# Kernel optimization log

Measured on AMD Instinct MI355X. Metric: run time of the kernel, lower is better.

## Reference

```python
import jax, jax.numpy as jnp
import numpy as np

B, T, D = 4, 8192, 1024
C = 8.0


def setup_inputs() -> dict:
    key = jax.random.key(0)
    k1, k2, k3 = jax.random.split(key, 3)
    init_std = D ** (-0.5)
    x = jax.random.normal(k1, (B, T, D), dtype=jnp.float32)
    W_in = jax.random.truncated_normal(k2, -3.0, 3.0, (D, D), dtype=jnp.float32) * init_std
    W_gate = jax.random.truncated_normal(k3, -3.0, 3.0, (D, D), dtype=jnp.float32) * init_std
    b_in = jnp.zeros((D,), dtype=jnp.float32)
    b_gate = jnp.zeros((D,), dtype=jnp.float32)
    forget_lambda = jnp.linspace(-4.323, -9.0, D, dtype=jnp.float32)
    return {"x": x, "W_in": W_in, "b_in": b_in, "W_gate": W_gate,
            "b_gate": b_gate, "forget_lambda": forget_lambda}


def _combine(c1, c2):
    # linear recurrence h_t = a_t * h_{t-1} + b_t  (associative composition)
    a1, b1 = c1
    a2, b2 = c2
    return a1 * a2, a2 * b1 + b2


def reference(x, W_in, b_in, W_gate, b_gate, forget_lambda):
    # x: [B, T, D]
    input_gate = x @ W_in.T + b_in          # [B, T, D]
    recurrence_gate = x @ W_gate.T + b_gate  # [B, T, D]
    alpha = jnp.exp(-C * jax.nn.softplus(forget_lambda) * jax.nn.sigmoid(recurrence_gate))
    beta = jnp.sqrt(1.0 - alpha ** 2 + 1e-6)
    xbeta = beta * jax.nn.sigmoid(input_gate) * x
    # parallel scan of h_t = alpha_t * h_{t-1} + xbeta_t along sequence axis
    _, h = jax.lax.associative_scan(_combine, (alpha, xbeta), axis=1)
    return h
```

## Files before the change

### kernel.cpp

```cpp
#include <hip/hip_runtime.h>

typedef unsigned short u16;
typedef __attribute__((ext_vector_type(8))) short short8;
typedef __attribute__((ext_vector_type(4))) float f32x4;

#define T_SEQ 8192
#define DDIM 1024
#define BB 4
#define MM (BB * T_SEQ)
#define NC 128
#define CHUNK (T_SEQ / NC)
#define CHAINS (BB * DDIM)
#define NT 16

__device__ __forceinline__ float bf_lo(unsigned p) {
    union { unsigned u; float f; } v; v.u = p << 16; return v.f;
}
__device__ __forceinline__ float bf_hi(unsigned p) {
    union { unsigned u; float f; } v; v.u = p & 0xffff0000u; return v.f;
}
__device__ __forceinline__ float bf_u16(u16 p) {
    union { unsigned u; float f; } v; v.u = ((unsigned)p) << 16; return v.f;
}
__device__ __forceinline__ u16 f2bf(float f) {
    union { unsigned u; float f; } v; v.f = f;
    unsigned r = v.u + 0x7fffu + ((v.u >> 16) & 1u);
    return (u16)(r >> 16);
}
__device__ __forceinline__ float sigm(float z) {
    return __builtin_amdgcn_rcpf(1.0f + __expf(-z));
}
__device__ __forceinline__ void gld16(const u16* g, u16* l) {
    __builtin_amdgcn_global_load_lds((const __attribute__((address_space(1))) void*)g,
                                     (__attribute__((address_space(3))) void*)l, 16, 0, 0);
}

#define N4X (MM * DDIM / 4)
#define N4W (DDIM * DDIM / 4)
__global__ __launch_bounds__(256) void cvt_all(const float* __restrict__ x,
                                               const float* __restrict__ Wi,
                                               const float* __restrict__ Wg,
                                               u16* __restrict__ Xb,
                                               u16* __restrict__ Wib,
                                               u16* __restrict__ Wgb) {
    int i = blockIdx.x * 256 + threadIdx.x;
    const float* src; u16* dst; int j;
    if (i < N4X)            { src = x;  dst = Xb;  j = i; }
    else if (i < N4X + N4W) { src = Wi; dst = Wib; j = i - N4X; }
    else                    { src = Wg; dst = Wgb; j = i - N4X - N4W; }
    float4 v = ((const float4*)src)[j];
    ushort4 o;
    o.x = f2bf(v.x); o.y = f2bf(v.y); o.z = f2bf(v.z); o.w = f2bf(v.w);
    ((ushort4*)dst)[j] = o;
}


#define MROW(i_, av)                                                                   \
    acc[i_][0] = __builtin_amdgcn_mfma_f32_16x16x32_bf16(av, b0, acc[i_][0], 0, 0, 0); \
    acc[i_][1] = __builtin_amdgcn_mfma_f32_16x16x32_bf16(av, b1, acc[i_][1], 0, 0, 0); \
    acc[i_][2] = __builtin_amdgcn_mfma_f32_16x16x32_bf16(av, b2, acc[i_][2], 0, 0, 0); \
    acc[i_][3] = __builtin_amdgcn_mfma_f32_16x16x32_bf16(av, b3, acc[i_][3], 0, 0, 0);

#define MALL MROW(0, a0) MROW(1, a1) MROW(2, a2) MROW(3, a3) \
             MROW(4, a4) MROW(5, a5) MROW(6, a6) MROW(7, a7)

#define RDALL(kk)                                                            \
    b0 = LDB(kk, 0); b1 = LDB(kk, 1); b2 = LDB(kk, 2); b3 = LDB(kk, 3);      \
    a0 = LDA(kk, 0); a1 = LDA(kk, 1); a2 = LDA(kk, 2); a3 = LDA(kk, 3);      \
    a4 = LDA(kk, 4); a5 = LDA(kk, 5); a6 = LDA(kk, 6); a7 = LDA(kk, 7);

#define STA(buf, kh, rb, t_) gld16(gA + (size_t)(t_)*64 + (kh)*32 + (size_t)(rb)*128*DDIM, \
                                   &lds[(((buf)*2 + (kh))*1024 + (rb)*512 + tid)*8])
#define STB(buf, kh, hf, t_) gld16(((hf) ? gBg : gBi) + (size_t)(t_)*64 + (kh)*32,          \
                                   &lds[32768 + (((buf)*2 + (kh))*1024 + (hf)*512 + tid)*8])

#define LDA(kk, i) (*(const short8*)&lds[((cur*2 + (kk))*256 + arow0 + (i)*16)*32 + aoff])
#define LDB(kk, j) (*(const short8*)&lds[32768 + ((cur*2 + (kk))*256 + brow0 + (j)*16)*32 + aoff])

__global__ __launch_bounds__(512, 2)
void gemm_fused(const u16* __restrict__ X, const u16* __restrict__ Wi,
                const u16* __restrict__ Wg, const float* __restrict__ b_in,
                const float* __restrict__ b_gate, const float* __restrict__ lam,
                u16* __restrict__ Sg, u16* __restrict__ XBg) {
    const int bid = blockIdx.x;
    const int xcd = bid & 7;
    const int r = bid >> 3;
    const int n_tile = r & 7;
    const int m_tile = xcd * 16 + (r >> 3);
    const int tN0 = n_tile * 128;
    const int tM0 = m_tile * 256;

    const int tid = threadIdx.x;
    const int lane = tid & 63;
    const int w = tid >> 6;
    const int wm = w >> 2;
    const int wn = w & 3;
    const int gate = wn >> 1;
    const int wn_sub = wn & 1;

    __shared__ u16 lds[65536];

    const int srow = tid >> 2;
    const int c8log = (tid & 3) ^ ((tid >> 3) & 3);
    const u16* gA  = X  + (size_t)(tM0 + srow) * DDIM + c8log * 8;
    const u16* gBi = Wi + (size_t)(tN0 + srow) * DDIM + c8log * 8;
    const u16* gBg = Wg + (size_t)(tN0 + srow) * DDIM + c8log * 8;

    const int lm = lane & 15;
    const int aoff = (((lane >> 4) ^ ((lm >> 1) & 3))) * 8;
    const int arow0 = wm * 128 + lm;
    const int brow0 = gate * 128 + wn_sub * 64 + lm;

    f32x4 acc[8][4] = {};
    short8 a0, a1, a2, a3, a4, a5, a6, a7, b0, b1, b2, b3;

    STA(0, 0, 0, 0); STA(0, 0, 1, 0); STB(0, 0, 0, 0); STB(0, 0, 1, 0);
    STA(0, 1, 0, 0); STA(0, 1, 1, 0); STB(0, 1, 0, 0); STB(0, 1, 1, 0);
    asm volatile("s_waitcnt vmcnt(4)" ::: "memory");
    __builtin_amdgcn_s_barrier();

    for (int t = 0; t < NT - 1; ++t) {
        const int cur = t & 1, nb = cur ^ 1, tn = t + 1;
        RDALL(0)
        STA(nb, 0, 0, tn); STA(nb, 0, 1, tn); STB(nb, 0, 0, tn); STB(nb, 0, 1, tn);
        asm volatile("s_waitcnt vmcnt(4)" ::: "memory");
        __builtin_amdgcn_s_barrier();
        __builtin_amdgcn_s_setprio(1);
        MALL
        __builtin_amdgcn_s_setprio(0);
        __builtin_amdgcn_s_barrier();
        RDALL(1)
        STA(nb, 1, 0, tn); STA(nb, 1, 1, tn); STB(nb, 1, 0, tn); STB(nb, 1, 1, tn);
        asm volatile("s_waitcnt vmcnt(4)" ::: "memory");
        __builtin_amdgcn_s_barrier();
        __builtin_amdgcn_s_setprio(1);
        MALL
        __builtin_amdgcn_s_setprio(0);
        __builtin_amdgcn_s_barrier();
    }
    {
        const int cur = (NT - 1) & 1;
        RDALL(0)
        asm volatile("s_waitcnt vmcnt(0)" ::: "memory");
        __builtin_amdgcn_s_barrier();
        __builtin_amdgcn_s_setprio(1);
        MALL
        __builtin_amdgcn_s_setprio(0);
        __builtin_amdgcn_s_barrier();
        RDALL(1)
        __builtin_amdgcn_s_setprio(1);
        MALL
        __builtin_amdgcn_s_setprio(0);
        __builtin_amdgcn_s_barrier();
    }

    const int r0 = (lane >> 4) << 2;
    const int cb = lane & 15;
    if (gate) {
#pragma unroll
        for (int j = 0; j < 4; ++j) {
            const int colg = tN0 + wn_sub * 64 + j * 16 + cb;
            const int cl = wn_sub * 64 + j * 16 + cb;
            const float bj = b_gate[colg];
            const float nsp = -8.0f * log1pf(__expf(lam[colg]));
#pragma unroll
            for (int i = 0; i < 8; ++i) {
                const int rl0 = wm * 128 + i * 16 + r0;
#pragma unroll
                for (int rr = 0; rr < 4; ++rr) {
                    const int rl = rl0 + rr;
                    float s = nsp * sigm(acc[i][j][rr] + bj);
                    lds[rl * 128 + (cl ^ (((rl >> 2) & 7) << 4))] = f2bf(s);
                }
            }
        }
    } else {
#pragma unroll
        for (int j = 0; j < 4; ++j) {
            const int colg = tN0 + wn_sub * 64 + j * 16 + cb;
            const int cl = wn_sub * 64 + j * 16 + cb;
            const float bj = b_in[colg];
#pragma unroll
            for (int i = 0; i < 8; ++i) {
                const int rl0 = wm * 128 + i * 16 + r0;
#pragma unroll
                for (int rr = 0; rr < 4; ++rr) {
                    const int rl = rl0 + rr;
                    float p = sigm(acc[i][j][rr] + bj);
                    lds[32768 + rl * 128 + (cl ^ (((rl >> 2) & 7) << 4))] =
                        (u16)(p * 65535.0f + 0.5f);
                }
            }
        }
    }
    asm volatile("s_waitcnt lgkmcnt(0)" ::: "memory");
    __builtin_amdgcn_s_barrier();
    __builtin_amdgcn_sched_barrier(0);

    const int cc = tid & 15;
    const int rg0 = (tid >> 4) * 8;
#pragma unroll
    for (int k = 0; k < 8; ++k) {
        const int rl = rg0 + k;
        const int ch = (cc ^ (((rl >> 2) & 7) << 1)) * 8;
        short8 sv = *(const short8*)&lds[rl * 128 + ch];
        short8 pv = *(const short8*)&lds[32768 + rl * 128 + ch];
        const size_t go = (size_t)(tM0 + rl) * DDIM + tN0 + cc * 8;
        short8 xv = *(const short8*)&X[go];
        short8 ov;
#pragma unroll
        for (int e = 0; e < 8; ++e) {
            float s = bf_u16((u16)sv[e]);
            float p = (float)((u16)pv[e]) * (1.0f / 65535.0f);
            float xf = bf_u16((u16)xv[e]);
            float be = sqrtf(1.0f - __expf(2.0f * s) + 1e-6f);
            ov[e] = (short)f2bf(be * p * xf);
        }
        *(short8*)&Sg[go] = sv;
        *(short8*)&XBg[go] = ov;
    }
}

__global__ __launch_bounds__(256)
void scan_pass1(const u16* __restrict__ S, const u16* __restrict__ XB,
                float* __restrict__ AggA, float* __restrict__ AggB) {
    const int c = blockIdx.x, dblk = blockIdx.y, bq = blockIdx.z;
    const int d0 = dblk * 512 + threadIdx.x * 2;
    size_t base = ((size_t)(bq * T_SEQ + c * CHUNK)) * DDIM + d0;

    float A0 = 1.0f, B0 = 0.0f, A1 = 1.0f, B1 = 0.0f;
#pragma unroll 8
    for (int t = 0; t < CHUNK; t++) {
        unsigned sp = *(const unsigned*)(S + base);
        unsigned xp = *(const unsigned*)(XB + base);
        float a0 = __expf(bf_lo(sp));
        float a1 = __expf(bf_hi(sp));
        B0 = fmaf(a0, B0, bf_lo(xp)); A0 *= a0;
        B1 = fmaf(a1, B1, bf_hi(xp)); A1 *= a1;
        base += DDIM;
    }
    const int chain = bq * DDIM + d0;
    float2 av; av.x = A0; av.y = A1;
    float2 bv; bv.x = B0; bv.y = B1;
    *(float2*)(AggA + (size_t)c * CHAINS + chain) = av;
    *(float2*)(AggB + (size_t)c * CHAINS + chain) = bv;
}

__global__ __launch_bounds__(256)
void scan_pass2(const float* __restrict__ AggA, const float* __restrict__ AggB,
                float* __restrict__ H0) {
    const int chain = blockIdx.x * 256 + threadIdx.x;
    float p = 0.0f;
#pragma unroll 8
    for (int c = 0; c < NC; c++) {
        H0[(size_t)c * CHAINS + chain] = p;
        p = AggA[(size_t)c * CHAINS + chain] * p + AggB[(size_t)c * CHAINS + chain];
    }
}

__global__ __launch_bounds__(256)
void scan_pass3(const u16* __restrict__ S, const u16* __restrict__ XB,
                const float* __restrict__ H0, float* __restrict__ out) {
    const int c = blockIdx.x, dblk = blockIdx.y, bq = blockIdx.z;
    const int d0 = dblk * 512 + threadIdx.x * 2;
    size_t base = ((size_t)(bq * T_SEQ + c * CHUNK)) * DDIM + d0;
    const int chain = bq * DDIM + d0;

    float2 h = *(const float2*)(H0 + (size_t)c * CHAINS + chain);
#pragma unroll 8
    for (int t = 0; t < CHUNK; t++) {
        unsigned sp = *(const unsigned*)(S + base);
        unsigned xp = *(const unsigned*)(XB + base);
        float a0 = __expf(bf_lo(sp));
        float a1 = __expf(bf_hi(sp));
        h.x = fmaf(a0, h.x, bf_lo(xp));
        h.y = fmaf(a1, h.y, bf_hi(xp));
        *(float2*)(out + base) = h;
        base += DDIM;
    }
}

extern "C" void kernel_launch(void* const* d_in, const int* in_sizes, int n_in,
                              void* d_out, int out_size, void* d_ws, size_t ws_size,
                              hipStream_t stream) {
    const float* x   = (const float*)d_in[0];
    const float* Win = (const float*)d_in[1];
    const float* bin = (const float*)d_in[2];
    const float* Wg  = (const float*)d_in[3];
    const float* bg  = (const float*)d_in[4];
    const float* lam = (const float*)d_in[5];
    float* out = (float*)d_out;

    char* w = (char*)d_ws;
    u16* Wi_bf  = (u16*)(w);
    u16* Wg_bf  = (u16*)(w + (size_t)(2) * 1024 * 1024);
    u16* Sg     = (u16*)(w + (size_t)(4) * 1024 * 1024);
    u16* XBg    = (u16*)(w + (size_t)(68) * 1024 * 1024);
    float* AggA = (float*)(w + (size_t)(132) * 1024 * 1024);
    float* AggB = (float*)(w + (size_t)(134) * 1024 * 1024);
    float* H0   = (float*)(w + (size_t)(136) * 1024 * 1024);

    u16* Xbf = (u16*)d_out;

    cvt_all<<<dim3((N4X + 2 * N4W) / 256), dim3(256), 0, stream>>>(
        x, Win, Wg, Xbf, Wi_bf, Wg_bf);

    gemm_fused<<<dim3((DDIM / 128) * (MM / 256)), dim3(512), 0, stream>>>(
        Xbf, Wi_bf, Wg_bf, bin, bg, lam, Sg, XBg);

    scan_pass1<<<dim3(NC, 2, BB), dim3(256), 0, stream>>>(Sg, XBg, AggA, AggB);
    scan_pass2<<<dim3(CHAINS / 256), dim3(256), 0, stream>>>(AggA, AggB, H0);
    scan_pass3<<<dim3(NC, 2, BB), dim3(256), 0, stream>>>(Sg, XBg, H0, out);
}
```

Before: 477.4 us.

## Restructure GEMM main loop into 4-stage half-tile LDS ring buffer with prefetch depth 3

Replaces the double-buffered 64-wide K-tile loop, which used two barriers per half-tile, with a 4-slot ring of 32-wide K half-tiles. Global loads run three stages ahead and each iteration needs only one barrier. This aims to hide more global-load latency and cut synchronisation overhead in the fused input/gate GEMM. The wait counts and slot reuse have to be exactly right, otherwise a slot could be overwritten while another wave is still reading it.

```diff
diff --git a/kernel.cpp b/kernel.cpp
--- a/kernel.cpp
+++ b/kernel.cpp
@@ -12,6 +12,7 @@
 #define CHUNK (T_SEQ / NC)
 #define CHAINS (BB * DDIM)
 #define NT 16
+#define NHT 32
 
 __device__ __forceinline__ float bf_lo(unsigned p) {
     union { unsigned u; float f; } v; v.u = p << 16; return v.f;
@@ -64,18 +65,19 @@
 #define MALL MROW(0, a0) MROW(1, a1) MROW(2, a2) MROW(3, a3) \
              MROW(4, a4) MROW(5, a5) MROW(6, a6) MROW(7, a7)
 
-#define RDALL(kk)                                                            \
-    b0 = LDB(kk, 0); b1 = LDB(kk, 1); b2 = LDB(kk, 2); b3 = LDB(kk, 3);      \
-    a0 = LDA(kk, 0); a1 = LDA(kk, 1); a2 = LDA(kk, 2); a3 = LDA(kk, 3);      \
-    a4 = LDA(kk, 4); a5 = LDA(kk, 5); a6 = LDA(kk, 6); a7 = LDA(kk, 7);
-
-#define STA(buf, kh, rb, t_) gld16(gA + (size_t)(t_)*64 + (kh)*32 + (size_t)(rb)*128*DDIM, \
-                                   &lds[(((buf)*2 + (kh))*1024 + (rb)*512 + tid)*8])
-#define STB(buf, kh, hf, t_) gld16(((hf) ? gBg : gBi) + (size_t)(t_)*64 + (kh)*32,          \
-                                   &lds[32768 + (((buf)*2 + (kh))*1024 + (hf)*512 + tid)*8])
-
-#define LDA(kk, i) (*(const short8*)&lds[((cur*2 + (kk))*256 + arow0 + (i)*16)*32 + aoff])
-#define LDB(kk, j) (*(const short8*)&lds[32768 + ((cur*2 + (kk))*256 + brow0 + (j)*16)*32 + aoff])
+#define LDA_H(h_, i) (*(const short8*)&lds[((h_)&3)*8192 + (arow0 + (i)*16)*32 + aoff])
+#define LDB_H(h_, j) (*(const short8*)&lds[32768 + ((h_)&3)*8192 + (brow0 + (j)*16)*32 + aoff])
+
+#define RD_H(h_)                                                                       \
+    b0 = LDB_H(h_, 0); b1 = LDB_H(h_, 1); b2 = LDB_H(h_, 2); b3 = LDB_H(h_, 3);        \
+    a0 = LDA_H(h_, 0); a1 = LDA_H(h_, 1); a2 = LDA_H(h_, 2); a3 = LDA_H(h_, 3);        \
+    a4 = LDA_H(h_, 4); a5 = LDA_H(h_, 5); a6 = LDA_H(h_, 6); a7 = LDA_H(h_, 7);
+
+#define STA_H(h_, rb) gld16(gA + (size_t)(h_)*32 + (size_t)(rb)*128*DDIM,              \
+                            &lds[((h_)&3)*8192 + (rb)*4096 + tid*8])
+#define STB_H(h_, hf) gld16(((hf) ? gBg : gBi) + (size_t)(h_)*32,                      \
+                            &lds[32768 + ((h_)&3)*8192 + (hf)*4096 + tid*8])
+#define ST_H(h_) STA_H(h_, 0); STA_H(h_, 1); STB_H(h_, 0); STB_H(h_, 1);
 
 __global__ __launch_bounds__(512, 2)
 void gemm_fused(const u16* __restrict__ X, const u16* __restrict__ Wi,
@@ -114,45 +116,42 @@
     f32x4 acc[8][4] = {};
     short8 a0, a1, a2, a3, a4, a5, a6, a7, b0, b1, b2, b3;
 
-    STA(0, 0, 0, 0); STA(0, 0, 1, 0); STB(0, 0, 0, 0); STB(0, 0, 1, 0);
-    STA(0, 1, 0, 0); STA(0, 1, 1, 0); STB(0, 1, 0, 0); STB(0, 1, 1, 0);
-    asm volatile("s_waitcnt vmcnt(4)" ::: "memory");
-    __builtin_amdgcn_s_barrier();
-
-    for (int t = 0; t < NT - 1; ++t) {
-        const int cur = t & 1, nb = cur ^ 1, tn = t + 1;
-        RDALL(0)
-        STA(nb, 0, 0, tn); STA(nb, 0, 1, tn); STB(nb, 0, 0, tn); STB(nb, 0, 1, tn);
-        asm volatile("s_waitcnt vmcnt(4)" ::: "memory");
+    ST_H(0) ST_H(1) ST_H(2)
+
+    for (int h = 0; h < NHT - 3; ++h) {
+        asm volatile("s_waitcnt vmcnt(8)" ::: "memory");
         __builtin_amdgcn_s_barrier();
+        RD_H(h)
+        ST_H(h + 3)
         __builtin_amdgcn_s_setprio(1);
         MALL
         __builtin_amdgcn_s_setprio(0);
+    }
+    {
+        asm volatile("s_waitcnt vmcnt(8)" ::: "memory");
         __builtin_amdgcn_s_barrier();
-        RDALL(1)
-        STA(nb, 1, 0, tn); STA(nb, 1, 1, tn); STB(nb, 1, 0, tn); STB(nb, 1, 1, tn);
-        asm volatile("s_waitcnt vmcnt(4)" ::: "memory");
-        __builtin_amdgcn_s_barrier();
+        RD_H(29)
         __builtin_amdgcn_s_setprio(1);
         MALL
         __builtin_amdgcn_s_setprio(0);
+    }
+    {
+        asm volatile("s_waitcnt vmcnt(4)" ::: "memory");
         __builtin_amdgcn_s_barrier();
-    }
-    {
-        const int cur = (NT - 1) & 1;
-        RDALL(0)
-        asm volatile("s_waitcnt vmcnt(0)" ::: "memory");
-        __builtin_amdgcn_s_barrier();
+        RD_H(30)
         __builtin_amdgcn_s_setprio(1);
         MALL
         __builtin_amdgcn_s_setprio(0);
+    }
+    {
+        asm volatile("s_waitcnt vmcnt(0)" ::: "memory");
         __builtin_amdgcn_s_barrier();
-        RDALL(1)
+        RD_H(31)
         __builtin_amdgcn_s_setprio(1);
         MALL
         __builtin_amdgcn_s_setprio(0);
-        __builtin_amdgcn_s_barrier();
-    }
+    }
+    __builtin_amdgcn_s_barrier();
 
     const int r0 = (lane >> 4) << 2;
     const int cb = lane & 15;
```

Result: no change. 474.4 us (-0.6%).
